# Kernel optimization log

Measured on AMD Instinct MI355X. Metric: run time of the kernel, lower is better.

The kernel has to match this reference:

```python
import jax, jax.numpy as jnp
import numpy as np
from math import exp

C1 = 0.01 ** 2
C2 = 0.03 ** 2
WINDOW_SIZE = 11
SIGMA = 1.5

def make_window(window_size, channel, sigma=SIGMA):
    g = np.array([exp(-(x - window_size // 2) ** 2 / float(2 * sigma ** 2))
                  for x in range(window_size)], dtype=np.float32)
    g = g / g.sum()
    w2d = np.outer(g, g).astype(np.float32)  # [ws, ws]
    # depthwise kernel, OIHW with I=1 per group: [C, 1, ws, ws]
    return jnp.asarray(np.broadcast_to(w2d, (channel, 1, window_size, window_size)).copy())

def depthwise_conv(x, window, pad):
    C = x.shape[1]
    return jax.lax.conv_general_dilated(
        x, window, window_strides=(1, 1),
        padding=[(pad, pad), (pad, pad)],
        feature_group_count=C,
        dimension_numbers=('NCHW', 'OIHW', 'NCHW'))

def setup_inputs() -> dict:
    key = jax.random.key(0)
    k1, k2 = jax.random.split(key)
    B, C, H, W = 16, 3, 512, 512
    img1 = jax.random.uniform(k1, (B, C, H, W), dtype=jnp.float32)
    img2 = jax.random.uniform(k2, (B, C, H, W), dtype=jnp.float32)
    window = make_window(WINDOW_SIZE, C)
    return {"img1": img1, "img2": img2, "window": window}

def reference(img1, img2, window):
    pad = WINDOW_SIZE // 2
    mu1 = depthwise_conv(img1, window, pad)
    mu2 = depthwise_conv(img2, window, pad)
    mu1_sq = mu1 * mu1
    mu2_sq = mu2 * mu2
    mu1_mu2 = mu1 * mu2
    sigma1_sq = depthwise_conv(img1 * img1, window, pad) - mu1_sq
    sigma2_sq = depthwise_conv(img2 * img2, window, pad) - mu2_sq
    sigma12 = depthwise_conv(img1 * img2, window, pad) - mu1_mu2
    ssim_cs = (2 * sigma12 + C2) / (sigma1_sq + sigma2_sq + C2)
    ssim_l = (2 * mu1_mu2 + C1) / (mu1_sq + mu2_sq + C1)
    ssim_map = ssim_l * ssim_cs
    return jnp.mean(ssim_map)
```

## Files before the change

kernel.cpp:

```cpp
#include <hip/hip_runtime.h>


#define IMG_H 512
#define IMG_W 512
#define N_IMG 48
#define WS 11
#define PAD 5
#define CHUNK 16
#define NCHUNK (IMG_H / CHUNK)
#define RING 12
#define OFF 6
#define VSW 524
#define INV_NPX (1.0f / (48.0f * 512.0f * 512.0f))

__global__ __launch_bounds__(256, 4) void ssim_partial_kernel(
    const float* __restrict__ img1,
    const float* __restrict__ img2,
    const float* __restrict__ window,
    float* __restrict__ out)
{
    __shared__ float vs[2][4][VSW];
    __shared__ float wred[4];

    const int tid = threadIdx.x;
    const int bc  = blockIdx.x;
    const int r0  = blockIdx.y * CHUNK;
    const int col = tid * 2;

    float g[WS];
    {
        const float g5  = sqrtf(window[5 * WS + 5]);
        const float inv = 1.0f / g5;
#pragma unroll
        for (int j = 0; j < WS; ++j) g[j] = window[5 * WS + j] * inv;
    }
    const float C1v = 0.01f * 0.01f;
    const float C2v = 0.03f * 0.03f;

    const float* __restrict__ p1 = img1 + (size_t)bc * (IMG_H * IMG_W);
    const float* __restrict__ p2 = img2 + (size_t)bc * (IMG_H * IMG_W);

    {
        float* vflat = &vs[0][0][0];
        for (int i = tid; i < 2 * 4 * VSW; i += 256) vflat[i] = 0.0f;
    }
    __syncthreads();

    float rx1a[RING], rx1b[RING], rx2a[RING], rx2b[RING];
#pragma unroll
    for (int i = 0; i < RING; ++i) { rx1a[i]=0.f; rx1b[i]=0.f; rx2a[i]=0.f; rx2b[i]=0.f; }

#pragma unroll
    for (int i = 0; i < 10; ++i) {
        const int rr = r0 - PAD + i;
        float a0=0.f, a1=0.f, b0=0.f, b1=0.f;
        if (rr >= 0 && rr < IMG_H) {
            const float2 u1 = *(const float2*)(p1 + rr * IMG_W + col);
            const float2 u2 = *(const float2*)(p2 + rr * IMG_W + col);
            a0 = u1.x; a1 = u1.y; b0 = u2.x; b1 = u2.y;
        }
        rx1a[2+i] = a0; rx1b[2+i] = a1; rx2a[2+i] = b0; rx2b[2+i] = b1;
    }

    float acc = 0.0f;

    for (int step = 0; step < CHUNK / 2; ++step) {
        const int R = r0 + step * 2;

#pragma unroll
        for (int i = 0; i < RING - 2; ++i) {
            rx1a[i] = rx1a[i+2]; rx1b[i] = rx1b[i+2];
            rx2a[i] = rx2a[i+2]; rx2b[i] = rx2b[i+2];
        }
#pragma unroll
        for (int j = 0; j < 2; ++j) {
            const int rr = R + PAD + j;
            float a0=0.f, a1=0.f, b0=0.f, b1=0.f;
            if (rr < IMG_H) {
                const float2 u1 = *(const float2*)(p1 + rr * IMG_W + col);
                const float2 u2 = *(const float2*)(p2 + rr * IMG_W + col);
                a0 = u1.x; a1 = u1.y; b0 = u2.x; b1 = u2.y;
            }
            rx1a[10+j] = a0; rx1b[10+j] = a1; rx2a[10+j] = b0; rx2b[10+j] = b1;
        }

#pragma unroll
        for (int j = 0; j < 2; ++j) {
            float v1a=0.f, v2a=0.f, vsa=0.f, vpa=0.f;
            float v1b=0.f, v2b=0.f, vsb=0.f, vpb=0.f;
#pragma unroll
            for (int i = 0; i < WS; ++i) {
                const float w  = g[i];
                const float x1 = rx1a[i+j], x2 = rx2a[i+j];
                const float t1 = w * x1,    t2 = w * x2;
                v1a += t1; v2a += t2;
                vsa = fmaf(t1, x1, fmaf(t2, x2, vsa));
                vpa = fmaf(t1, x2, vpa);
                const float y1 = rx1b[i+j], y2 = rx2b[i+j];
                const float s1 = w * y1,    s2 = w * y2;
                v1b += s1; v2b += s2;
                vsb = fmaf(s1, y1, fmaf(s2, y2, vsb));
                vpb = fmaf(s1, y2, vpb);
            }
            *(float2*)&vs[j][0][OFF + col] = make_float2(v1a, v1b);
            *(float2*)&vs[j][1][OFF + col] = make_float2(v2a, v2b);
            *(float2*)&vs[j][2][OFF + col] = make_float2(vsa, vsb);
            *(float2*)&vs[j][3][OFF + col] = make_float2(vpa, vpb);
        }
        __syncthreads();

#pragma unroll
        for (int j = 0; j < 2; ++j) {
            float hv[2][4];
#pragma unroll
            for (int p = 0; p < 4; ++p) {
                const float2* q = (const float2*)&vs[j][p][col];
                const float2 f0=q[0], f1=q[1], f2=q[2], f3=q[3],
                             f4=q[4], f5=q[5], f6=q[6];
                const float b[14] = {f0.x,f0.y,f1.x,f1.y,f2.x,f2.y,f3.x,f3.y,
                                     f4.x,f4.y,f5.x,f5.y,f6.x,f6.y};
                float s0 = 0.f, s1 = 0.f;
#pragma unroll
                for (int i = 0; i < WS; ++i) {
                    s0 = fmaf(g[i], b[i+1], s0);
                    s1 = fmaf(g[i], b[i+2], s1);
                }
                hv[0][p] = s0; hv[1][p] = s1;
            }
#pragma unroll
            for (int k = 0; k < 2; ++k) {
                const float mu1 = hv[k][0], mu2 = hv[k][1];
                const float hs  = hv[k][2], hp  = hv[k][3];
                const float mu1s = mu1 * mu1;
                const float mu2s = mu2 * mu2;
                const float mu12 = mu1 * mu2;
                const float sgs  = hs - mu1s - mu2s;
                const float sg12 = hp - mu12;
                const float num  = (2.f * mu12 + C1v) * (2.f * sg12 + C2v);
                const float den  = (mu1s + mu2s + C1v) * (sgs + C2v);
                float r = __builtin_amdgcn_rcpf(den);
                r = r * fmaf(-den, r, 2.0f);
                acc = fmaf(num, r, acc);
            }
        }
        __syncthreads();
    }

#pragma unroll
    for (int off = 32; off > 0; off >>= 1)
        acc += __shfl_down(acc, off);
    if ((tid & 63) == 0) wred[tid >> 6] = acc;
    __syncthreads();
    if (tid == 0) {
        const float s = (wred[0] + wred[1]) + (wred[2] + wred[3]);
        atomicAdd(out, s * INV_NPX);
    }
}

extern "C" void kernel_launch(void* const* d_in, const int* in_sizes, int n_in,
                              void* d_out, int out_size, void* d_ws, size_t ws_size,
                              hipStream_t stream) {
    const float* img1   = (const float*)d_in[0];
    const float* img2   = (const float*)d_in[1];
    const float* window = (const float*)d_in[2];
    float* out = (float*)d_out;

    hipMemsetAsync(out, 0, sizeof(float), stream);
    dim3 grid(N_IMG, NCHUNK);
    ssim_partial_kernel<<<grid, 256, 0, stream>>>(img1, img2, window, out);
}
```

Baseline: 155.8 us.

## Pack row pairs into float2 vectors with swizzled LDS layout for packed FMA

Rewrites the vertical and horizontal passes on ext_vector float2 so the compiler can emit packed FP32 FMA (v_pk_fma_f32), processing two output rows per instruction. The LDS intermediate is relaid out so each element holds the values for both rows, with an XOR-free pad swizzle (8 bytes every 8 elements) to avoid bank conflicts, and only the halo cells are zeroed instead of the whole buffer. The occupancy hint in launch_bounds is dropped. Packing the row-pair results requires extra register shuffles, and removing the min-blocks hint may change register allocation and occupancy.

Result: faster. 146.6 us (-5.9%).

```diff
diff --git a/kernel.cpp b/kernel.cpp
--- a/kernel.cpp
+++ b/kernel.cpp
@@ -1,5 +1,7 @@
 #include <hip/hip_runtime.h>
 
+
+typedef float v2f __attribute__((ext_vector_type(2)));
 
 #define IMG_H 512
 #define IMG_W 512
@@ -9,18 +11,24 @@
 #define CHUNK 16
 #define NCHUNK (IMG_H / CHUNK)
 #define RING 12
-#define OFF 6
-#define VSW 524
+#define PLANE_B 4736
 #define INV_NPX (1.0f / (48.0f * 512.0f * 512.0f))
 
-__global__ __launch_bounds__(256, 4) void ssim_partial_kernel(
+__device__ __forceinline__ unsigned swz(int E) { return 8u * E + 8u * (E >> 3); }
+
+__device__ __forceinline__ v2f vfma(v2f a, v2f b, v2f c) {
+    return __builtin_elementwise_fma(a, b, c);
+}
+
+__global__ __launch_bounds__(256) void ssim_partial_kernel(
     const float* __restrict__ img1,
     const float* __restrict__ img2,
     const float* __restrict__ window,
     float* __restrict__ out)
 {
-    __shared__ float vs[2][4][VSW];
+    __shared__ __align__(16) char lds[4 * PLANE_B];
     __shared__ float wred[4];
+#define LDSE(p, off) (*(v2f*)(lds + (p) * PLANE_B + (off)))
 
     const int tid = threadIdx.x;
     const int bc  = blockIdx.x;
@@ -40,26 +48,32 @@
     const float* __restrict__ p1 = img1 + (size_t)bc * (IMG_H * IMG_W);
     const float* __restrict__ p2 = img2 + (size_t)bc * (IMG_H * IMG_W);
 
-    {
-        float* vflat = &vs[0][0][0];
-        for (int i = tid; i < 2 * 4 * VSW; i += 256) vflat[i] = 0.0f;
+    unsigned roff[12];
+#pragma unroll
+    for (int m = 0; m < 12; ++m) roff[m] = swz(2 * tid + 1 + m);
+    const unsigned woffA = swz(2 * tid + 6);
+    const unsigned woffB = swz(2 * tid + 7);
+
+    for (int i = tid; i < 48; i += 256) {
+        const int p = i / 12, h = i % 12;
+        const int E = (h < 6) ? h : (512 + h);
+        LDSE(p, swz(E)) = (v2f)(0.0f);
     }
     __syncthreads();
 
-    float rx1a[RING], rx1b[RING], rx2a[RING], rx2b[RING];
+    v2f rx1[RING], rx2[RING];
 #pragma unroll
-    for (int i = 0; i < RING; ++i) { rx1a[i]=0.f; rx1b[i]=0.f; rx2a[i]=0.f; rx2b[i]=0.f; }
+    for (int i = 0; i < RING; ++i) { rx1[i] = (v2f)(0.0f); rx2[i] = (v2f)(0.0f); }
 
 #pragma unroll
     for (int i = 0; i < 10; ++i) {
         const int rr = r0 - PAD + i;
-        float a0=0.f, a1=0.f, b0=0.f, b1=0.f;
+        v2f u1 = (v2f)(0.0f), u2 = (v2f)(0.0f);
         if (rr >= 0 && rr < IMG_H) {
-            const float2 u1 = *(const float2*)(p1 + rr * IMG_W + col);
-            const float2 u2 = *(const float2*)(p2 + rr * IMG_W + col);
-            a0 = u1.x; a1 = u1.y; b0 = u2.x; b1 = u2.y;
+            u1 = *(const v2f*)(p1 + rr * IMG_W + col);
+            u2 = *(const v2f*)(p2 + rr * IMG_W + col);
         }
-        rx1a[2+i] = a0; rx1b[2+i] = a1; rx2a[2+i] = b0; rx2b[2+i] = b1;
+        rx1[2 + i] = u1; rx2[2 + i] = u2;
     }
 
     float acc = 0.0f;
@@ -68,80 +82,75 @@
         const int R = r0 + step * 2;
 
 #pragma unroll
-        for (int i = 0; i < RING - 2; ++i) {
-            rx1a[i] = rx1a[i+2]; rx1b[i] = rx1b[i+2];
-            rx2a[i] = rx2a[i+2]; rx2b[i] = rx2b[i+2];
-        }
+        for (int i = 0; i < RING - 2; ++i) { rx1[i] = rx1[i + 2]; rx2[i] = rx2[i + 2]; }
 #pragma unroll
         for (int j = 0; j < 2; ++j) {
             const int rr = R + PAD + j;
-            float a0=0.f, a1=0.f, b0=0.f, b1=0.f;
+            v2f u1 = (v2f)(0.0f), u2 = (v2f)(0.0f);
             if (rr < IMG_H) {
-                const float2 u1 = *(const float2*)(p1 + rr * IMG_W + col);
-                const float2 u2 = *(const float2*)(p2 + rr * IMG_W + col);
-                a0 = u1.x; a1 = u1.y; b0 = u2.x; b1 = u2.y;
+                u1 = *(const v2f*)(p1 + rr * IMG_W + col);
+                u2 = *(const v2f*)(p2 + rr * IMG_W + col);
             }
-            rx1a[10+j] = a0; rx1b[10+j] = a1; rx2a[10+j] = b0; rx2b[10+j] = b1;
+            rx1[10 + j] = u1; rx2[10 + j] = u2;
         }
 
+        v2f a1_0 = (v2f)(0.f), a2_0 = (v2f)(0.f), aS_0 = (v2f)(0.f), aP_0 = (v2f)(0.f);
+        v2f a1_1 = (v2f)(0.f), a2_1 = (v2f)(0.f), aS_1 = (v2f)(0.f), aP_1 = (v2f)(0.f);
 #pragma unroll
-        for (int j = 0; j < 2; ++j) {
-            float v1a=0.f, v2a=0.f, vsa=0.f, vpa=0.f;
-            float v1b=0.f, v2b=0.f, vsb=0.f, vpb=0.f;
+        for (int i = 0; i < WS; ++i) {
+            const float w = g[i];
+            {
+                const v2f X1 = rx1[i], X2 = rx2[i];
+                a1_0 = vfma((v2f)(w), X1, a1_0);
+                a2_0 = vfma((v2f)(w), X2, a2_0);
+                aS_0 = vfma((v2f)(w), vfma(X1, X1, X2 * X2), aS_0);
+                aP_0 = vfma((v2f)(w), X1 * X2, aP_0);
+            }
+            {
+                const v2f X1 = rx1[i + 1], X2 = rx2[i + 1];
+                a1_1 = vfma((v2f)(w), X1, a1_1);
+                a2_1 = vfma((v2f)(w), X2, a2_1);
+                aS_1 = vfma((v2f)(w), vfma(X1, X1, X2 * X2), aS_1);
+                aP_1 = vfma((v2f)(w), X1 * X2, aP_1);
+            }
+        }
+        LDSE(0, woffA) = (v2f){a1_0.x, a1_1.x}; LDSE(0, woffB) = (v2f){a1_0.y, a1_1.y};
+        LDSE(1, woffA) = (v2f){a2_0.x, a2_1.x}; LDSE(1, woffB) = (v2f){a2_0.y, a2_1.y};
+        LDSE(2, woffA) = (v2f){aS_0.x, aS_1.x}; LDSE(2, woffB) = (v2f){aS_0.y, aS_1.y};
+        LDSE(3, woffA) = (v2f){aP_0.x, aP_1.x}; LDSE(3, woffB) = (v2f){aP_0.y, aP_1.y};
+        __syncthreads();
+
+        v2f hA[4], hB[4];
+#pragma unroll
+        for (int p = 0; p < 4; ++p) {
+            v2f r[12];
+#pragma unroll
+            for (int m = 0; m < 12; ++m) r[m] = LDSE(p, roff[m]);
+            v2f sA = (v2f)(0.f), sB = (v2f)(0.f);
 #pragma unroll
             for (int i = 0; i < WS; ++i) {
-                const float w  = g[i];
-                const float x1 = rx1a[i+j], x2 = rx2a[i+j];
-                const float t1 = w * x1,    t2 = w * x2;
-                v1a += t1; v2a += t2;
-                vsa = fmaf(t1, x1, fmaf(t2, x2, vsa));
-                vpa = fmaf(t1, x2, vpa);
-                const float y1 = rx1b[i+j], y2 = rx2b[i+j];
-                const float s1 = w * y1,    s2 = w * y2;
-                v1b += s1; v2b += s2;
-                vsb = fmaf(s1, y1, fmaf(s2, y2, vsb));
-                vpb = fmaf(s1, y2, vpb);
+                sA = vfma((v2f)(g[i]), r[i],     sA);
+                sB = vfma((v2f)(g[i]), r[i + 1], sB);
             }
-            *(float2*)&vs[j][0][OFF + col] = make_float2(v1a, v1b);
-            *(float2*)&vs[j][1][OFF + col] = make_float2(v2a, v2b);
-            *(float2*)&vs[j][2][OFF + col] = make_float2(vsa, vsb);
-            *(float2*)&vs[j][3][OFF + col] = make_float2(vpa, vpb);
+            hA[p] = sA; hB[p] = sB;
         }
-        __syncthreads();
-
 #pragma unroll
-        for (int j = 0; j < 2; ++j) {
-            float hv[2][4];
-#pragma unroll
-            for (int p = 0; p < 4; ++p) {
-                const float2* q = (const float2*)&vs[j][p][col];
-                const float2 f0=q[0], f1=q[1], f2=q[2], f3=q[3],
-                             f4=q[4], f5=q[5], f6=q[6];
-                const float b[14] = {f0.x,f0.y,f1.x,f1.y,f2.x,f2.y,f3.x,f3.y,
-                                     f4.x,f4.y,f5.x,f5.y,f6.x,f6.y};
-                float s0 = 0.f, s1 = 0.f;
-#pragma unroll
-                for (int i = 0; i < WS; ++i) {
-                    s0 = fmaf(g[i], b[i+1], s0);
-                    s1 = fmaf(g[i], b[i+2], s1);
-                }
-                hv[0][p] = s0; hv[1][p] = s1;
-            }
-#pragma unroll
-            for (int k = 0; k < 2; ++k) {
-                const float mu1 = hv[k][0], mu2 = hv[k][1];
-                const float hs  = hv[k][2], hp  = hv[k][3];
-                const float mu1s = mu1 * mu1;
-                const float mu2s = mu2 * mu2;
-                const float mu12 = mu1 * mu2;
-                const float sgs  = hs - mu1s - mu2s;
-                const float sg12 = hp - mu12;
-                const float num  = (2.f * mu12 + C1v) * (2.f * sg12 + C2v);
-                const float den  = (mu1s + mu2s + C1v) * (sgs + C2v);
-                float r = __builtin_amdgcn_rcpf(den);
-                r = r * fmaf(-den, r, 2.0f);
-                acc = fmaf(num, r, acc);
-            }
+        for (int k = 0; k < 2; ++k) {
+            const v2f mu1 = k ? hB[0] : hA[0];
+            const v2f mu2 = k ? hB[1] : hA[1];
+            const v2f hs  = k ? hB[2] : hA[2];
+            const v2f hp  = k ? hB[3] : hA[3];
+            const v2f mu1s = mu1 * mu1;
+            const v2f mu2s = mu2 * mu2;
+            const v2f mu12 = mu1 * mu2;
+            const v2f sgs  = hs - mu1s - mu2s;
+            const v2f sg12 = hp - mu12;
+            const v2f num  = (2.f * mu12 + (v2f)(C1v)) * (2.f * sg12 + (v2f)(C2v));
+            const v2f den  = (mu1s + mu2s + (v2f)(C1v)) * (sgs + (v2f)(C2v));
+            v2f r = {__builtin_amdgcn_rcpf(den.x), __builtin_amdgcn_rcpf(den.y)};
+            r = r * vfma(-den, r, (v2f)(2.0f));
+            acc = fmaf(num.x, r.x, acc);
+            acc = fmaf(num.y, r.y, acc);
         }
         __syncthreads();
     }
```
